# Performance work log

Hardware: AMD Instinct MI355X
Metric: run time of the kernel (lower is better)

Reference implementation:

```python
import jax, jax.numpy as jnp
from jax import lax
import numpy as np

EMBED, HIDDEN, VOCAB = 512, 512, 10000
ATT, ENC = 512, 2048
B, NPIX, T = 128, 49, 30


def _lin(k, out_d, in_d):
    k1, k2 = jax.random.split(k)
    s = 1.0 / np.sqrt(in_d)
    return (jax.random.uniform(k1, (out_d, in_d), minval=-s, maxval=s),
            jax.random.uniform(k2, (out_d,), minval=-s, maxval=s))


def setup_inputs() -> dict:
    key = jax.random.key(0)
    ks = jax.random.split(key, 24)
    inp = {}
    inp['enc_image'] = jax.random.normal(ks[0], (B, NPIX, ENC))
    inp['global_features'] = jax.random.normal(ks[1], (B, ENC))
    inp['encoded_captions'] = jax.random.randint(ks[2], (B, T), 0, VOCAB)
    lens = jax.random.randint(ks[3], (B,), 1, T + 1).at[0].set(T)
    inp['caption_lengths'] = lens[:, None]
    # parameters
    inp['emb_W'] = jax.random.uniform(ks[4], (VOCAB, EMBED), minval=-0.1, maxval=0.1)
    inp['e2h_W'], inp['e2h_b'] = _lin(ks[5], HIDDEN, ENC)
    inp['gf_W'], inp['gf_b'] = _lin(ks[6], EMBED, ENC)
    inp['fc_W'] = jax.random.uniform(ks[7], (VOCAB, HIDDEN), minval=-0.1, maxval=0.1)
    inp['fc_b'] = jnp.zeros((VOCAB,))
    inp['lstm_Wih'], inp['lstm_bih'] = _lin(ks[8], 4 * HIDDEN, 2 * EMBED)
    inp['lstm_Whh'], inp['lstm_bhh'] = _lin(ks[9], 4 * HIDDEN, HIDDEN)
    inp['xg_W'], inp['xg_b'] = _lin(ks[10], HIDDEN, 2 * EMBED)
    inp['hg_W'], inp['hg_b'] = _lin(ks[11], HIDDEN, HIDDEN)
    inp['senaff_W'], inp['senaff_b'] = _lin(ks[12], HIDDEN, HIDDEN)
    inp['senatt_W'], inp['senatt_b'] = _lin(ks[13], ATT, HIDDEN)
    inp['haff_W'], inp['haff_b'] = _lin(ks[14], HIDDEN, HIDDEN)
    inp['hatt_W'], inp['hatt_b'] = _lin(ks[15], ATT, HIDDEN)
    inp['vatt_W'], inp['vatt_b'] = _lin(ks[16], ATT, HIDDEN)
    inp['alph_W'], inp['alph_b'] = _lin(ks[17], 1, ATT)
    inp['ctx_W'], inp['ctx_b'] = _lin(ks[18], HIDDEN, HIDDEN)
    return inp


def reference(enc_image, global_features, encoded_captions, caption_lengths,
              emb_W, e2h_W, e2h_b, gf_W, gf_b, fc_W, fc_b,
              lstm_Wih, lstm_bih, lstm_Whh, lstm_bhh,
              xg_W, xg_b, hg_W, hg_b,
              senaff_W, senaff_b, senatt_W, senatt_b,
              haff_W, haff_b, hatt_W, hatt_b,
              vatt_W, vatt_b, alph_W, alph_b, ctx_W, ctx_b):
    lengths = caption_lengths[:, 0]
    order = jnp.argsort(-lengths)                     # descending (stable)
    lengths = lengths[order]
    spatial = jax.nn.relu(jnp.einsum('bpe,he->bph', enc_image[order], e2h_W) + e2h_b)  # (B,NP,H)
    gimg = jax.nn.relu(global_features[order] @ gf_W.T + gf_b)                          # (B,E)
    embs = emb_W[encoded_captions[order]]                                               # (B,T,E)
    inputs = jnp.concatenate([embs, jnp.broadcast_to(gimg[:, None, :], embs.shape)], axis=-1)  # (B,T,2E)
    vattn = jnp.einsum('bph,ah->bpa', spatial, vatt_W) + vatt_b                         # (B,NP,A) hoisted
    h0 = jnp.zeros((spatial.shape[0], HIDDEN), spatial.dtype)
    c0 = h0

    def step(carry, xs):
        h, c = carry
        xt, mask = xs                                  # (B,2E), (B,) bool = row still active
        gates = xt @ lstm_Wih.T + lstm_bih + h @ lstm_Whh.T + lstm_bhh
        i, f, g, o = jnp.split(gates, 4, axis=-1)
        c_new = jax.nn.sigmoid(f) * c + jax.nn.sigmoid(i) * jnp.tanh(g)
        h_new = jax.nn.sigmoid(o) * jnp.tanh(c_new)
        st = jax.nn.sigmoid(xt @ xg_W.T + xg_b + h @ hg_W.T + hg_b) * jnp.tanh(c_new)  # sentinel
        sen_aff = jax.nn.relu(st @ senaff_W.T + senaff_b)    # (B,H)
        sen_att = sen_aff @ senatt_W.T + senatt_b            # (B,A)
        h_aff = jnp.tanh(h_new @ haff_W.T + haff_b)
        h_att = h_aff @ hatt_W.T + hatt_b
        att_feats = jnp.concatenate([vattn, sen_att[:, None, :]], axis=1)   # (B,NP+1,A)
        scores = jnp.tanh(att_feats + h_att[:, None, :]) @ alph_W[0] + alph_b[0]
        alpha = jax.nn.softmax(scores, axis=1)               # (B,NP+1)
        cat_feats = jnp.concatenate([spatial, sen_aff[:, None, :]], axis=1)
        context = jnp.einsum('bph,bp->bh', cat_feats, alpha)
        out_l = jnp.tanh((context + h_aff) @ ctx_W.T + ctx_b)
        pt = out_l @ fc_W.T + fc_b                           # dropout = identity (eval)
        m = mask[:, None]
        return (jnp.where(m, h_new, h), jnp.where(m, c_new, c)), jnp.where(m, pt, 0.0)

    masks = lengths[None, :] > jnp.arange(T)[:, None]        # (T,B) replicates shrinking batch_size_t
    _, preds = lax.scan(step, (h0, c0), (jnp.swapaxes(inputs, 0, 1), masks))
    return jnp.swapaxes(preds, 0, 1)                         # (B,T,VOCAB), sorted-by-length order
```

## Files before the change

kernel.cpp:

```cpp
#include <hip/hip_runtime.h>
#include <hip/hip_bf16.h>
#include <cstdint>
#include <cstddef>

#define DEVI __device__ __forceinline__

#define BB 128
#define TT 30
#define VOCAB 10000
#define ENCD 2048
#define NPIX 49
#define SLOT 65536

typedef __attribute__((ext_vector_type(8))) short bf16x8;
typedef __attribute__((ext_vector_type(4))) float f32x4;

DEVI float bf2f(unsigned short u){ union{float f; unsigned int i;} x; x.i=((unsigned)u)<<16; return x.f; }
DEVI unsigned short f2bf(float f){ union{float f; unsigned int i;} x; x.f=f; unsigned r=x.i + 0x7fffu + ((x.i>>16)&1u); return (unsigned short)(r>>16); }
DEVI float sigm(float x){ return 1.0f/(1.0f+expf(-x)); }
DEVI f32x4 mfma16(bf16x8 a, bf16x8 b, f32x4 c){ return __builtin_amdgcn_mfma_f32_16x16x32_bf16(a,b,c,0,0,0); }

DEVI uint4 byp16(const void* p){
  const unsigned long long* q=(const unsigned long long*)p;
  unsigned long long a=__hip_atomic_load(q,   __ATOMIC_RELAXED, __HIP_MEMORY_SCOPE_AGENT);
  unsigned long long b=__hip_atomic_load(q+1, __ATOMIC_RELAXED, __HIP_MEMORY_SCOPE_AGENT);
  uint4 r; r.x=(unsigned)a; r.y=(unsigned)(a>>32); r.z=(unsigned)b; r.w=(unsigned)(b>>32); return r;
}
DEVI unsigned byp4(const void* p){
  return __hip_atomic_load((const unsigned*)p, __ATOMIC_RELAXED, __HIP_MEMORY_SCOPE_AGENT);
}

DEVI void waitflags(int* flags, int thresh){
  __syncthreads();
  if(threadIdx.x < 64){
    for(;;){
      int v = (threadIdx.x<32) ? __hip_atomic_load(&flags[threadIdx.x], __ATOMIC_RELAXED, __HIP_MEMORY_SCOPE_AGENT)
                               : 0x7fffffff;
      if(__all(v >= thresh)) break;
      __builtin_amdgcn_s_sleep(1);
    }
  }
  asm volatile("" ::: "memory");
  __syncthreads();
}
DEVI void signal(int* flag, int val){
  __syncthreads();
  if(threadIdx.x==0) __hip_atomic_store(flag, val, __ATOMIC_RELEASE, __HIP_MEMORY_SCOPE_AGENT);
}

__global__ void k_sort(const int* __restrict__ lens, int* __restrict__ order, int* __restrict__ Bt){
  __shared__ int L[BB];
  int i = threadIdx.x;
  L[i] = lens[i];
  __syncthreads();
  int li = L[i]; int rank = 0;
  for(int j=0;j<BB;j++){ int lj=L[j]; rank += (lj>li) || (lj==li && j<i); }
  order[rank] = i;
  if(i<TT){ int c=0; for(int j=0;j<BB;j++) c += (L[j]>i); Bt[i]=c; }
}

struct WC13 { const float* src[13]; unsigned short* dst[13]; int n[13]; };
__global__ void k_wconv(WC13 wc){
  int stride = gridDim.x*blockDim.x;
  int tid0 = blockIdx.x*blockDim.x + threadIdx.x;
  for(int s=0;s<13;s++){
    const float4* src=(const float4*)wc.src[s];
    int n4 = wc.n[s]>>2;
    ushort4* dst=(ushort4*)wc.dst[s];
    for(int i=tid0;i<n4;i+=stride){
      float4 v=src[i];
      ushort4 o; o.x=f2bf(v.x); o.y=f2bf(v.y); o.z=f2bf(v.z); o.w=f2bf(v.w);
      dst[i]=o;
    }
  }
}

__global__ void k_xt(const int* __restrict__ caps, const int* __restrict__ order,
                     const float* __restrict__ embW, const unsigned short* __restrict__ gimg,
                     unsigned short* __restrict__ xt){
  int total=BB*TT*1024;
  for(int idx=blockIdx.x*blockDim.x+threadIdx.x; idx<total; idx+=gridDim.x*blockDim.x){
    int k=idx&1023; int bt=idx>>10; int t=bt%TT; int b=bt/TT;
    unsigned short v;
    if(k<512){ int tok=caps[order[b]*TT+t]; v=f2bf(embW[(size_t)tok*512+k]); }
    else v=gimg[b*512+(k-512)];
    xt[idx]=v;
  }
}

__global__ __launch_bounds__(256) void k_gemm_f32A2(
    const float* __restrict__ A, int lda, int rpb, const int* __restrict__ order,
    const unsigned short* __restrict__ W, const float* __restrict__ bias,
    unsigned short* __restrict__ out, int K)
{
  __shared__ unsigned short As[128][136];
  int tid=threadIdx.x, wave=tid>>6, lane=tid&63, l15=lane&15, l4=lane>>4;
  int mb = blockIdx.y*128;
  f32x4 acc[8][4];
  f32x4 z = {0.f,0.f,0.f,0.f};
  #pragma unroll
  for(int i=0;i<8;i++)
    #pragma unroll
    for(int j=0;j<4;j++) acc[i][j]=z;
  int cch=tid&15, r0=tid>>4;
  int nb = blockIdx.x*256 + wave*64;
  for(int kc=0;kc<K;kc+=128){
    __syncthreads();
    #pragma unroll
    for(int rp=0;rp<8;rp++){
      int r=r0+rp*16;
      int m=mb+r;
      int sb = order[m/rpb]*rpb + m%rpb;
      const float* p = A + (size_t)sb*lda + kc + cch*8;
      float4 v0=*(const float4*)p, v1=*(const float4*)(p+4);
      unsigned short* d=&As[r][cch*8];
      d[0]=f2bf(v0.x); d[1]=f2bf(v0.y); d[2]=f2bf(v0.z); d[3]=f2bf(v0.w);
      d[4]=f2bf(v1.x); d[5]=f2bf(v1.y); d[6]=f2bf(v1.z); d[7]=f2bf(v1.w);
    }
    __syncthreads();
    #pragma unroll
    for(int kk=0;kk<4;kk++){
      bf16x8 bfr[4];
      #pragma unroll
      for(int nt=0;nt<4;nt++)
        bfr[nt] = *(const bf16x8*)(W + (size_t)(nb+nt*16+l15)*K + kc + kk*32 + l4*8);
      #pragma unroll
      for(int mt=0;mt<8;mt++){
        bf16x8 af = *(const bf16x8*)&As[mt*16+l15][kk*32+l4*8];
        #pragma unroll
        for(int nt=0;nt<4;nt++) acc[mt][nt]=mfma16(af,bfr[nt],acc[mt][nt]);
      }
    }
  }
  #pragma unroll
  for(int nt=0;nt<4;nt++){
    int n = nb + nt*16 + l15;
    float bs = bias[n];
    #pragma unroll
    for(int mt=0;mt<8;mt++){
      #pragma unroll
      for(int j=0;j<4;j++){
        int row = mb + mt*16 + l4*4 + j;
        float v = acc[mt][nt][j]+bs; v = v>0.f ? v : 0.f;
        out[(size_t)row*512 + n] = f2bf(v);
      }
    }
  }
}

template<int BYP>
DEVI void dev_gemm512(unsigned short (*As)[136], const unsigned short* A, const unsigned short* W,
                      const float* bias, unsigned short* out, int act, int xtile, int mb){
  int tid=threadIdx.x, wave=tid>>6, lane=tid&63, l15=lane&15, l4=lane>>4;
  f32x4 acc[8];
  f32x4 z = {0.f,0.f,0.f,0.f};
  #pragma unroll
  for(int i=0;i<8;i++) acc[i]=z;
  int cch=tid&15, r0=tid>>4;
  int nrow = xtile*64 + wave*16 + l15;
  for(int kc=0;kc<512;kc+=128){
    __syncthreads();
    #pragma unroll
    for(int rp=0;rp<8;rp++){
      int r=r0+rp*16;
      const unsigned short* src = A + (size_t)(mb+r)*512 + kc + cch*8;
      if(BYP) *(uint4*)&As[r][cch*8] = byp16(src);
      else    *(uint4*)&As[r][cch*8] = *(const uint4*)src;
    }
    __syncthreads();
    #pragma unroll
    for(int kk=0;kk<4;kk++){
      bf16x8 bfr = *(const bf16x8*)(W + (size_t)nrow*512 + kc + kk*32 + l4*8);
      #pragma unroll
      for(int mt=0;mt<8;mt++){
        bf16x8 af = *(const bf16x8*)&As[mt*16+l15][kk*32+l4*8];
        acc[mt]=mfma16(af,bfr,acc[mt]);
      }
    }
  }
  float bs = bias ? bias[nrow] : 0.f;
  #pragma unroll
  for(int mt=0;mt<8;mt++){
    #pragma unroll
    for(int j=0;j<4;j++){
      int row = mb + mt*16 + l4*4 + j;
      float v = acc[mt][j]+bs;
      if(act==1) v = fmaxf(v,0.f);
      else if(act==2) v = tanhf(v);
      out[(size_t)row*512+nrow]=f2bf(v);
    }
  }
  __syncthreads();
}

struct PreD { const unsigned short* A; const unsigned short* W; const float* bias; unsigned short* out; };
struct PreD2 { PreD d[2]; };
__global__ __launch_bounds__(256) void k_pre(PreD2 dd){
  __shared__ unsigned short As[128][136];
  PreD g = dd.d[blockIdx.z];
  dev_gemm512<0>(As, g.A, g.W, g.bias, g.out, 0, blockIdx.x, blockIdx.y*128);
}

struct PCtx {
  const unsigned short *xt, *w_ih, *w_hh, *w_xg, *w_hg;
  const unsigned short *w_saff, *w_satt, *w_haff, *w_hatt, *w_ctx, *w_fc;
  const unsigned short *vattn, *SC;
  const float *bih,*bhh,*bxg,*bhg, *sab,*stbias,*hab,*htb, *alW,*alb, *cxb, *fcb;
  const int *Bt;
  unsigned short *h_hist;
  unsigned short *stb;
  unsigned short *tbuf;
  float *dout;
  int *Lflag;
  int *Tflag;
};

DEVI void dev_lstm(unsigned short (*As)[136], const PCtx& p, int t, int jblk,
                   const unsigned short* hprev, unsigned short* hout, float creg[2][4]){
  int tid=threadIdx.x, wave=tid>>6, lane=tid&63, l15=lane&15, l4=lane>>4;
  int jb = jblk*16;
  f32x4 acc[2][5];
  f32x4 z = {0.f,0.f,0.f,0.f};
  #pragma unroll
  for(int m=0;m<2;m++)
    #pragma unroll
    for(int s=0;s<5;s++) acc[m][s]=z;
  int cch=tid&15, r0=tid>>4;
  for(int kc=0;kc<1536;kc+=128){
    __syncthreads();
    #pragma unroll
    for(int rp=0;rp<8;rp++){
      int r=r0+rp*16;
      int kg = kc + cch*8;
      if(kg<1024){
        *(uint4*)&As[r][cch*8] = *(const uint4*)(p.xt + (size_t)r*(TT*1024) + t*1024 + kg);
      } else {
        *(uint4*)&As[r][cch*8] = byp16(hprev + (size_t)r*512 + (kg-1024));
      }
    }
    __syncthreads();
    #pragma unroll
    for(int kk=0;kk<4;kk++){
      int kg = kc + kk*32 + l4*8;
      bf16x8 bfr[5];
      #pragma unroll
      for(int s=0;s<5;s++){
        int row = (s<4) ? (s*512 + jb + l15) : (jb + l15);
        const unsigned short* wp;
        if(s<4) wp = (kg<1024) ? (p.w_ih + (size_t)row*1024 + kg) : (p.w_hh + (size_t)row*512 + (kg-1024));
        else    wp = (kg<1024) ? (p.w_xg + (size_t)row*1024 + kg) : (p.w_hg + (size_t)row*512 + (kg-1024));
        bfr[s] = *(const bf16x8*)wp;
      }
      #pragma unroll
      for(int m=0;m<2;m++){
        int mt = wave*2+m;
        bf16x8 af = *(const bf16x8*)&As[mt*16+l15][kk*32+l4*8];
        #pragma unroll
        for(int s=0;s<5;s++) acc[m][s]=mfma16(af,bfr[s],acc[m][s]);
      }
    }
  }
  int bt = p.Bt[t];
  int j = jb + l15;
  float bi  = p.bih[j]      + p.bhh[j];
  float bff = p.bih[512+j]  + p.bhh[512+j];
  float bg  = p.bih[1024+j] + p.bhh[1024+j];
  float bo  = p.bih[1536+j] + p.bhh[1536+j];
  float bs  = p.bxg[j] + p.bhg[j];
  unsigned short* stt = p.stb + (size_t)t*SLOT;
  #pragma unroll
  for(int m=0;m<2;m++){
    int mt = wave*2+m;
    #pragma unroll
    for(int jj=0;jj<4;jj++){
      int b = mt*16 + l4*4 + jj;
      float iv = sigm(acc[m][0][jj]+bi);
      float fv = sigm(acc[m][1][jj]+bff);
      float gv = tanhf(acc[m][2][jj]+bg);
      float ov = sigm(acc[m][3][jj]+bo);
      float sv = sigm(acc[m][4][jj]+bs);
      float cn = fv*creg[m][jj] + iv*gv;
      float tc = tanhf(cn);
      size_t idx=(size_t)b*512+j;
      if(b<bt){ hout[idx]=f2bf(ov*tc); creg[m][jj]=cn; }
      else {
        unsigned pr = byp4(hprev + (idx & ~(size_t)1));
        hout[idx] = (j&1) ? (unsigned short)(pr>>16) : (unsigned short)pr;
      }
      stt[idx]=f2bf(sv*tc);
    }
  }
}

DEVI void dev_attn(float* sS, float* sA, int b, const PCtx& p,
                   const unsigned short* satt, const unsigned short* hatt,
                   const unsigned short* scs, const unsigned short* sch,
                   unsigned short* outl){
  int tid=threadIdx.x; int gid=tid>>4, gl=tid&15;
  const unsigned short* ha = hatt + (size_t)b*512;
  #pragma unroll
  for(int rp=0;rp<4;rp++){
    int pp = rp*16 + gid;
    float s = 0.f;
    if(pp<50){
      const unsigned short* vp = p.vattn + ((size_t)b*NPIX + pp)*512;
      const unsigned short* sa = satt + (size_t)b*512;
      #pragma unroll 4
      for(int kk=0;kk<16;kk++){
        int k = gl*32 + kk*2;
        unsigned hu = byp4(ha + k);
        float h0=bf2f((unsigned short)hu), h1=bf2f((unsigned short)(hu>>16));
        float a0,a1;
        if(pp<NPIX){ a0=bf2f(vp[k]); a1=bf2f(vp[k+1]); }
        else { unsigned su=byp4(sa + k); a0=bf2f((unsigned short)su); a1=bf2f((unsigned short)(su>>16)); }
        s += tanhf(a0+h0)*p.alW[k] + tanhf(a1+h1)*p.alW[k+1];
      }
    }
    #pragma unroll
    for(int off=8;off>=1;off>>=1) s += __shfl_xor(s, off);
    if(gl==0 && pp<50) sS[pp] = s + p.alb[0];
  }
  __syncthreads();
  if(tid<64){
    float sv = (tid<50) ? sS[tid] : -1e30f;
    float m = sv;
    #pragma unroll
    for(int off=32;off>=1;off>>=1) m = fmaxf(m, __shfl_xor(m, off));
    float e = (tid<50) ? expf(sv-m) : 0.f;
    float sum = e;
    #pragma unroll
    for(int off=32;off>=1;off>>=1) sum += __shfl_xor(sum, off);
    if(tid<50) sA[tid] = e/sum;
  }
  __syncthreads();
  float a49 = sA[49];
  {
    int n0 = tid*2;
    unsigned schU = byp4(sch + (size_t)b*512 + n0);
    unsigned scsU = byp4(scs + (size_t)b*512 + n0);
    float acc0 = bf2f((unsigned short)schU) + a49*bf2f((unsigned short)(schU>>16))*0.f;
    float c0 = bf2f((unsigned short)schU), c1 = bf2f((unsigned short)(schU>>16));
    float s0 = bf2f((unsigned short)scsU), s1 = bf2f((unsigned short)(scsU>>16));
    acc0 = c0 + a49*s0 + p.cxb[n0];
    float acc1 = c1 + a49*s1 + p.cxb[n0+1];
    const unsigned short* sp = p.SC + (size_t)b*NPIX*512 + n0;
    for(int pp=0;pp<NPIX;pp++){
      unsigned u = *(const unsigned*)(sp + (size_t)pp*512);
      acc0 += sA[pp]*bf2f((unsigned short)u);
      acc1 += sA[pp]*bf2f((unsigned short)(u>>16));
    }
    unsigned o = ((unsigned)f2bf(tanhf(acc1))<<16) | (unsigned)f2bf(tanhf(acc0));
    *(unsigned*)(outl + (size_t)b*512 + n0) = o;
  }
  __syncthreads();
}

DEVI void dev_fc(unsigned short (*As)[136], const PCtx& p, int t, int xtile,
                 const unsigned short* outl){
  int tid=threadIdx.x, wave=tid>>6, lane=tid&63, l15=lane&15, l4=lane>>4;
  int bt = p.Bt[t];
  f32x4 acc[8];
  f32x4 z = {0.f,0.f,0.f,0.f};
  #pragma unroll
  for(int i=0;i<8;i++) acc[i]=z;
  int cch=tid&15, r0=tid>>4;
  int nbase = xtile*64 + wave*16;
  int nr = nbase + l15; if(nr > VOCAB-1) nr = VOCAB-1;
  for(int kc=0;kc<512;kc+=128){
    __syncthreads();
    #pragma unroll
    for(int rp=0;rp<8;rp++){
      int r=r0+rp*16;
      *(uint4*)&As[r][cch*8] = byp16(outl + (size_t)r*512 + kc + cch*8);
    }
    __syncthreads();
    #pragma unroll
    for(int kk=0;kk<4;kk++){
      bf16x8 bfr = *(const bf16x8*)(p.w_fc + (size_t)nr*512 + kc + kk*32 + l4*8);
      #pragma unroll
      for(int mt=0;mt<8;mt++){
        if(mt*16 < bt){
          bf16x8 af = *(const bf16x8*)&As[mt*16+l15][kk*32+l4*8];
          acc[mt]=mfma16(af,bfr,acc[mt]);
        }
      }
    }
  }
  int n = nbase + l15; bool nok = n < VOCAB;
  float bs = nok ? p.fcb[n] : 0.f;
  #pragma unroll
  for(int mt=0;mt<8;mt++){
    #pragma unroll
    for(int j=0;j<4;j++){
      int b = mt*16 + l4*4 + j;
      float v = (b<bt) ? (acc[mt][j]+bs) : 0.f;
      if(nok) p.dout[(size_t)b*(TT*VOCAB) + (size_t)t*VOCAB + n] = v;
    }
  }
  __syncthreads();
}

__global__ __launch_bounds__(256) void k_persist(PCtx p){
  __shared__ unsigned short As[128][136];
  __shared__ float sS[52];
  __shared__ float sA[52];
  int cb = blockIdx.x;
  if(cb < 32){
    float creg[2][4];
    #pragma unroll
    for(int m=0;m<2;m++)
      #pragma unroll
      for(int j=0;j<4;j++) creg[m][j]=0.f;
    for(int t=0;t<TT;t++){
      if(t>0) waitflags(p.Lflag, t);
      dev_lstm(As, p, t, cb, p.h_hist + (size_t)t*SLOT, p.h_hist + (size_t)(t+1)*SLOT, creg);
      signal(&p.Lflag[cb], t+1);
    }
  } else {
    int team = (cb-32)>>5, w = (cb-32)&31;
    unsigned short* S = p.tbuf + (size_t)team*7*SLOT;
    unsigned short *Saff=S, *Haff=S+SLOT, *Outl=S+2*SLOT, *Satt=S+3*SLOT,
                   *Hatt=S+4*SLOT, *Scs=S+5*SLOT, *Sch=S+6*SLOT;
    int* tf = p.Tflag + team*32;
    int it=0;
    for(int t=team; t<TT; t+=7, it++){
      waitflags(p.Lflag, t+1);
      if(w<8)       dev_gemm512<1>(As, p.stb + (size_t)t*SLOT,        p.w_saff, p.sab, Saff, 1, w,   0);
      else if(w<16) dev_gemm512<1>(As, p.h_hist + (size_t)(t+1)*SLOT, p.w_haff, p.hab, Haff, 2, w-8, 0);
      signal(&tf[w], it*3+1); waitflags(tf, it*3+1);
      if(w<8)       dev_gemm512<1>(As, Saff, p.w_satt, p.stbias, Satt, 0, w,    0);
      else if(w<16) dev_gemm512<1>(As, Haff, p.w_hatt, p.htb,    Hatt, 0, w-8,  0);
      else if(w<24) dev_gemm512<1>(As, Saff, p.w_ctx,  nullptr,  Scs,  0, w-16, 0);
      else          dev_gemm512<1>(As, Haff, p.w_ctx,  nullptr,  Sch,  0, w-24, 0);
      signal(&tf[w], it*3+2); waitflags(tf, it*3+2);
      for(int r=0;r<4;r++) dev_attn(sS, sA, w*4+r, p, Satt, Hatt, Scs, Sch, Outl);
      signal(&tf[w], it*3+3); waitflags(tf, it*3+3);
      for(int x=w; x<157; x+=32) dev_fc(As, p, t, x, Outl);
    }
  }
}

extern "C" void kernel_launch(void* const* d_in, const int* in_sizes, int n_in,
                              void* d_out, int out_size, void* d_ws, size_t ws_size,
                              hipStream_t stream)
{
  const float* enc  =(const float*)d_in[0];
  const float* gfeat=(const float*)d_in[1];
  const int*   caps =(const int*)d_in[2];
  const int*   lens =(const int*)d_in[3];
  const float* embW =(const float*)d_in[4];
  const float* e2hW =(const float*)d_in[5];  const float* e2hb=(const float*)d_in[6];
  const float* gfW  =(const float*)d_in[7];  const float* gfb =(const float*)d_in[8];
  const float* fcW  =(const float*)d_in[9];  const float* fcb =(const float*)d_in[10];
  const float* WihF =(const float*)d_in[11]; const float* bih =(const float*)d_in[12];
  const float* WhhF =(const float*)d_in[13]; const float* bhh =(const float*)d_in[14];
  const float* xgWF =(const float*)d_in[15]; const float* bxg =(const float*)d_in[16];
  const float* hgWF =(const float*)d_in[17]; const float* bhg =(const float*)d_in[18];
  const float* saWF =(const float*)d_in[19]; const float* sab =(const float*)d_in[20];
  const float* stWF =(const float*)d_in[21]; const float* stbias=(const float*)d_in[22];
  const float* haWF =(const float*)d_in[23]; const float* hab =(const float*)d_in[24];
  const float* htWF =(const float*)d_in[25]; const float* htb =(const float*)d_in[26];
  const float* vaWF =(const float*)d_in[27]; const float* vab =(const float*)d_in[28];
  const float* alW  =(const float*)d_in[29]; const float* alb =(const float*)d_in[30];
  const float* cxWF =(const float*)d_in[31]; const float* cxb =(const float*)d_in[32];

  char* base=(char*)d_ws; size_t off=0;
  auto alloc=[&](size_t bytes)->void*{ void* r=base+off; off += (bytes+255)&~(size_t)255; return r; };

  int* order=(int*)alloc(BB*4);
  int* Bt   =(int*)alloc(32*4);
  unsigned short* w_e2h =(unsigned short*)alloc((size_t)512*2048*2);
  unsigned short* w_gf  =(unsigned short*)alloc((size_t)512*2048*2);
  unsigned short* w_fc  =(unsigned short*)alloc((size_t)VOCAB*512*2);
  unsigned short* w_ih  =(unsigned short*)alloc((size_t)2048*1024*2);
  unsigned short* w_hh  =(unsigned short*)alloc((size_t)2048*512*2);
  unsigned short* w_xg  =(unsigned short*)alloc((size_t)512*1024*2);
  unsigned short* w_hg  =(unsigned short*)alloc((size_t)512*512*2);
  unsigned short* w_saff=(unsigned short*)alloc((size_t)512*512*2);
  unsigned short* w_satt=(unsigned short*)alloc((size_t)512*512*2);
  unsigned short* w_haff=(unsigned short*)alloc((size_t)512*512*2);
  unsigned short* w_hatt=(unsigned short*)alloc((size_t)512*512*2);
  unsigned short* w_vatt=(unsigned short*)alloc((size_t)512*512*2);
  unsigned short* w_ctx =(unsigned short*)alloc((size_t)512*512*2);
  unsigned short* spatial=(unsigned short*)alloc((size_t)BB*NPIX*512*2);
  unsigned short* vattn  =(unsigned short*)alloc((size_t)BB*NPIX*512*2);
  unsigned short* SC     =(unsigned short*)alloc((size_t)BB*NPIX*512*2);
  unsigned short* gimg   =(unsigned short*)alloc((size_t)BB*512*2);
  unsigned short* xt     =(unsigned short*)alloc((size_t)BB*TT*1024*2);
  int* flags =(int*)alloc(4096);
  unsigned short* tbuf=(unsigned short*)alloc((size_t)7*7*SLOT*2);

  unsigned short* stb_hist = w_e2h;
  unsigned short* h_hist   = spatial;

  k_sort<<<1,BB,0,stream>>>(lens, order, Bt);

  WC13 wc;
  const float* srcs[13] = {e2hW,gfW,fcW,WihF,WhhF,xgWF,hgWF,saWF,stWF,haWF,htWF,vaWF,cxWF};
  unsigned short* dsts[13] = {w_e2h,w_gf,w_fc,w_ih,w_hh,w_xg,w_hg,w_saff,w_satt,w_haff,w_hatt,w_vatt,w_ctx};
  int ns[13] = {512*2048,512*2048,VOCAB*512,2048*1024,2048*512,512*1024,512*512,512*512,512*512,512*512,512*512,512*512,512*512};
  for(int i=0;i<13;i++){ wc.src[i]=srcs[i]; wc.dst[i]=dsts[i]; wc.n[i]=ns[i]; }
  k_wconv<<<1024,256,0,stream>>>(wc);

  k_gemm_f32A2<<<dim3(2,NPIX),256,0,stream>>>(enc, ENCD, NPIX, order, w_e2h, e2hb, spatial, ENCD);
  k_gemm_f32A2<<<dim3(2,1),  256,0,stream>>>(gfeat, ENCD, 1, order, w_gf, gfb, gimg, ENCD);
  k_xt<<<1024,256,0,stream>>>(caps, order, embW, gimg, xt);
  {
    PreD2 dv{};
    dv.d[0] = PreD{spatial, w_vatt, vab,     vattn};
    dv.d[1] = PreD{spatial, w_ctx,  nullptr, SC};
    k_pre<<<dim3(8,NPIX,2),256,0,stream>>>(dv);
  }

  hipMemsetAsync(h_hist, 0, (size_t)SLOT*2, stream);
  hipMemsetAsync(flags, 0, 4096, stream);

  PCtx pc;
  pc.xt=xt; pc.w_ih=w_ih; pc.w_hh=w_hh; pc.w_xg=w_xg; pc.w_hg=w_hg;
  pc.w_saff=w_saff; pc.w_satt=w_satt; pc.w_haff=w_haff; pc.w_hatt=w_hatt; pc.w_ctx=w_ctx; pc.w_fc=w_fc;
  pc.vattn=vattn; pc.SC=SC;
  pc.bih=bih; pc.bhh=bhh; pc.bxg=bxg; pc.bhg=bhg;
  pc.sab=sab; pc.stbias=stbias; pc.hab=hab; pc.htb=htb;
  pc.alW=alW; pc.alb=alb; pc.cxb=cxb; pc.fcb=fcb;
  pc.Bt=Bt;
  pc.h_hist=h_hist; pc.stb=stb_hist; pc.tbuf=tbuf;
  pc.dout=(float*)d_out;
  pc.Lflag=flags; pc.Tflag=flags+64;

  k_persist<<<256,256,0,stream>>>(pc);
}
```

Measured before the change: 2.403 ms.

## Cut polling contention with single done flag; stage full FC activations in LDS

```diff
diff --git a/kernel.cpp b/kernel.cpp
--- a/kernel.cpp
+++ b/kernel.cpp
@@ -37,7 +37,7 @@
       int v = (threadIdx.x<32) ? __hip_atomic_load(&flags[threadIdx.x], __ATOMIC_RELAXED, __HIP_MEMORY_SCOPE_AGENT)
                                : 0x7fffffff;
       if(__all(v >= thresh)) break;
-      __builtin_amdgcn_s_sleep(1);
+      __builtin_amdgcn_s_sleep(8);
     }
   }
   asm volatile("" ::: "memory");
@@ -46,6 +46,19 @@
 DEVI void signal(int* flag, int val){
   __syncthreads();
   if(threadIdx.x==0) __hip_atomic_store(flag, val, __ATOMIC_RELEASE, __HIP_MEMORY_SCOPE_AGENT);
+}
+DEVI void waitdone(int* f, int thresh){
+  __syncthreads();
+  if(threadIdx.x==0){
+    int spins=0;
+    while(__hip_atomic_load(f, __ATOMIC_RELAXED, __HIP_MEMORY_SCOPE_AGENT) < thresh){
+      if(spins<8) __builtin_amdgcn_s_sleep(4);
+      else        __builtin_amdgcn_s_sleep(64);
+      spins++;
+    }
+  }
+  asm volatile("" ::: "memory");
+  __syncthreads();
 }
 
 __global__ void k_sort(const int* __restrict__ lens, int* __restrict__ order, int* __restrict__ Bt){
@@ -212,6 +225,7 @@
   unsigned short *tbuf;
   float *dout;
   int *Lflag;
+  int *Ldone;
   int *Tflag;
 };
 
@@ -292,28 +306,26 @@
   }
 }
 
-DEVI void dev_attn(float* sS, float* sA, int b, const PCtx& p,
+DEVI void dev_attn(float* sS, float* sA, unsigned short* sHA, unsigned short* sSA,
+                   int b, const PCtx& p,
                    const unsigned short* satt, const unsigned short* hatt,
                    const unsigned short* scs, const unsigned short* sch,
                    unsigned short* outl){
-  int tid=threadIdx.x; int gid=tid>>4, gl=tid&15;
-  const unsigned short* ha = hatt + (size_t)b*512;
+  int tid=threadIdx.x;
+  if(tid<64)       *(uint4*)&sHA[tid*8] = byp16(hatt + (size_t)b*512 + tid*8);
+  else if(tid<128){ int q=tid-64; *(uint4*)&sSA[q*8] = byp16(satt + (size_t)b*512 + q*8); }
+  __syncthreads();
+  int gid=tid>>4, gl=tid&15;
   #pragma unroll
   for(int rp=0;rp<4;rp++){
     int pp = rp*16 + gid;
     float s = 0.f;
     if(pp<50){
-      const unsigned short* vp = p.vattn + ((size_t)b*NPIX + pp)*512;
-      const unsigned short* sa = satt + (size_t)b*512;
-      #pragma unroll 4
-      for(int kk=0;kk<16;kk++){
-        int k = gl*32 + kk*2;
-        unsigned hu = byp4(ha + k);
-        float h0=bf2f((unsigned short)hu), h1=bf2f((unsigned short)(hu>>16));
-        float a0,a1;
-        if(pp<NPIX){ a0=bf2f(vp[k]); a1=bf2f(vp[k+1]); }
-        else { unsigned su=byp4(sa + k); a0=bf2f((unsigned short)su); a1=bf2f((unsigned short)(su>>16)); }
-        s += tanhf(a0+h0)*p.alW[k] + tanhf(a1+h1)*p.alW[k+1];
+      if(pp<NPIX){
+        const unsigned short* vp = p.vattn + ((size_t)b*NPIX + pp)*512;
+        for(int k=gl*32;k<gl*32+32;k++) s += tanhf(bf2f(vp[k]) + bf2f(sHA[k])) * p.alW[k];
+      } else {
+        for(int k=gl*32;k<gl*32+32;k++) s += tanhf(bf2f(sSA[k]) + bf2f(sHA[k])) * p.alW[k];
       }
     }
     #pragma unroll
@@ -338,10 +350,9 @@
     int n0 = tid*2;
     unsigned schU = byp4(sch + (size_t)b*512 + n0);
     unsigned scsU = byp4(scs + (size_t)b*512 + n0);
-    float acc0 = bf2f((unsigned short)schU) + a49*bf2f((unsigned short)(schU>>16))*0.f;
     float c0 = bf2f((unsigned short)schU), c1 = bf2f((unsigned short)(schU>>16));
     float s0 = bf2f((unsigned short)scsU), s1 = bf2f((unsigned short)(scsU>>16));
-    acc0 = c0 + a49*s0 + p.cxb[n0];
+    float acc0 = c0 + a49*s0 + p.cxb[n0];
     float acc1 = c1 + a49*s1 + p.cxb[n0+1];
     const unsigned short* sp = p.SC + (size_t)b*NPIX*512 + n0;
     for(int pp=0;pp<NPIX;pp++){
@@ -355,55 +366,60 @@
   __syncthreads();
 }
 
-DEVI void dev_fc(unsigned short (*As)[136], const PCtx& p, int t, int xtile,
-                 const unsigned short* outl){
-  int tid=threadIdx.x, wave=tid>>6, lane=tid&63, l15=lane&15, l4=lane>>4;
+DEVI void dev_fc_all(unsigned short (*As2)[520], const PCtx& p, int t, int w,
+                     const unsigned short* outl){
+  int tid=threadIdx.x;
+  __syncthreads();
+  #pragma unroll
+  for(int i=0;i<32;i++){
+    int idx = i*256 + tid;
+    int r = idx>>6, c = (idx&63)<<3;
+    *(uint4*)&As2[r][c] = byp16(outl + (size_t)r*512 + c);
+  }
+  __syncthreads();
+  int wave=tid>>6, lane=tid&63, l15=lane&15, l4=lane>>4;
   int bt = p.Bt[t];
-  f32x4 acc[8];
-  f32x4 z = {0.f,0.f,0.f,0.f};
-  #pragma unroll
-  for(int i=0;i<8;i++) acc[i]=z;
-  int cch=tid&15, r0=tid>>4;
-  int nbase = xtile*64 + wave*16;
-  int nr = nbase + l15; if(nr > VOCAB-1) nr = VOCAB-1;
-  for(int kc=0;kc<512;kc+=128){
-    __syncthreads();
-    #pragma unroll
-    for(int rp=0;rp<8;rp++){
-      int r=r0+rp*16;
-      *(uint4*)&As[r][cch*8] = byp16(outl + (size_t)r*512 + kc + cch*8);
-    }
-    __syncthreads();
-    #pragma unroll
-    for(int kk=0;kk<4;kk++){
-      bf16x8 bfr = *(const bf16x8*)(p.w_fc + (size_t)nr*512 + kc + kk*32 + l4*8);
+  for(int x=w; x<157; x+=32){
+    f32x4 acc[8];
+    f32x4 z = {0.f,0.f,0.f,0.f};
+    #pragma unroll
+    for(int i=0;i<8;i++) acc[i]=z;
+    int nbase = x*64 + wave*16;
+    int nr = nbase + l15; if(nr > VOCAB-1) nr = VOCAB-1;
+    #pragma unroll 4
+    for(int kk=0;kk<16;kk++){
+      bf16x8 bfr = *(const bf16x8*)(p.w_fc + (size_t)nr*512 + kk*32 + l4*8);
       #pragma unroll
       for(int mt=0;mt<8;mt++){
         if(mt*16 < bt){
-          bf16x8 af = *(const bf16x8*)&As[mt*16+l15][kk*32+l4*8];
+          bf16x8 af = *(const bf16x8*)&As2[mt*16+l15][kk*32+l4*8];
           acc[mt]=mfma16(af,bfr,acc[mt]);
         }
       }
     }
-  }
-  int n = nbase + l15; bool nok = n < VOCAB;
-  float bs = nok ? p.fcb[n] : 0.f;
-  #pragma unroll
-  for(int mt=0;mt<8;mt++){
-    #pragma unroll
-    for(int j=0;j<4;j++){
-      int b = mt*16 + l4*4 + j;
-      float v = (b<bt) ? (acc[mt][j]+bs) : 0.f;
-      if(nok) p.dout[(size_t)b*(TT*VOCAB) + (size_t)t*VOCAB + n] = v;
+    int n = nbase + l15; bool nok = n < VOCAB;
+    float bs = nok ? p.fcb[n] : 0.f;
+    #pragma unroll
+    for(int mt=0;mt<8;mt++){
+      #pragma unroll
+      for(int j=0;j<4;j++){
+        int b = mt*16 + l4*4 + j;
+        float v = (b<bt) ? (acc[mt][j]+bs) : 0.f;
+        if(nok) p.dout[(size_t)b*(TT*VOCAB) + (size_t)t*VOCAB + n] = v;
+      }
     }
   }
   __syncthreads();
 }
 
 __global__ __launch_bounds__(256) void k_persist(PCtx p){
-  __shared__ unsigned short As[128][136];
-  __shared__ float sS[52];
-  __shared__ float sA[52];
+  __shared__ __align__(16) char smem[133760];
+  auto As  = (unsigned short (*)[136])smem;
+  auto As2 = (unsigned short (*)[520])smem;
+  float* sS = (float*)(smem + 133120);
+  float* sA = sS + 52;
+  unsigned short* sHA = (unsigned short*)smem;
+  unsigned short* sSA = sHA + 512;
   int cb = blockIdx.x;
   if(cb < 32){
     float creg[2][4];
@@ -412,9 +428,18 @@
       #pragma unroll
       for(int j=0;j<4;j++) creg[m][j]=0.f;
     for(int t=0;t<TT;t++){
-      if(t>0) waitflags(p.Lflag, t);
+      if(t>0){
+        waitflags(p.Lflag, t);
+        if(cb==0 && threadIdx.x==0)
+          __hip_atomic_store(p.Ldone, t, __ATOMIC_RELEASE, __HIP_MEMORY_SCOPE_AGENT);
+      }
       dev_lstm(As, p, t, cb, p.h_hist + (size_t)t*SLOT, p.h_hist + (size_t)(t+1)*SLOT, creg);
       signal(&p.Lflag[cb], t+1);
+    }
+    if(cb==0){
+      waitflags(p.Lflag, TT);
+      if(threadIdx.x==0)
+        __hip_atomic_store(p.Ldone, TT, __ATOMIC_RELEASE, __HIP_MEMORY_SCOPE_AGENT);
     }
   } else {
     int team = (cb-32)>>5, w = (cb-32)&31;
@@ -424,7 +449,7 @@
     int* tf = p.Tflag + team*32;
     int it=0;
     for(int t=team; t<TT; t+=7, it++){
-      waitflags(p.Lflag, t+1);
+      waitdone(p.Ldone, t+1);
       if(w<8)       dev_gemm512<1>(As, p.stb + (size_t)t*SLOT,        p.w_saff, p.sab, Saff, 1, w,   0);
       else if(w<16) dev_gemm512<1>(As, p.h_hist + (size_t)(t+1)*SLOT, p.w_haff, p.hab, Haff, 2, w-8, 0);
       signal(&tf[w], it*3+1); waitflags(tf, it*3+1);
@@ -433,9 +458,9 @@
       else if(w<24) dev_gemm512<1>(As, Saff, p.w_ctx,  nullptr,  Scs,  0, w-16, 0);
       else          dev_gemm512<1>(As, Haff, p.w_ctx,  nullptr,  Sch,  0, w-24, 0);
       signal(&tf[w], it*3+2); waitflags(tf, it*3+2);
-      for(int r=0;r<4;r++) dev_attn(sS, sA, w*4+r, p, Satt, Hatt, Scs, Sch, Outl);
+      for(int r=0;r<4;r++) dev_attn(sS, sA, sHA, sSA, w*4+r, p, Satt, Hatt, Scs, Sch, Outl);
       signal(&tf[w], it*3+3); waitflags(tf, it*3+3);
-      for(int x=w; x<157; x+=32) dev_fc(As, p, t, x, Outl);
+      dev_fc_all(As2, p, t, w, Outl);
     }
   }
 }
@@ -525,7 +550,7 @@
   pc.Bt=Bt;
   pc.h_hist=h_hist; pc.stb=stb_hist; pc.tbuf=tbuf;
   pc.dout=(float*)d_out;
-  pc.Lflag=flags; pc.Tflag=flags+64;
+  pc.Lflag=flags; pc.Ldone=flags+32; pc.Tflag=flags+64;
 
   k_persist<<<256,256,0,stream>>>(pc);
 }
```

After: 2.290 ms. 4.7% less time.
